# Optimization experiments

Hardware: AMD Instinct MI355X
Metric: run time of the kernel (lower is better)

## Reference

```python
import jax, jax.numpy as jnp
import numpy as np
from jax import lax

SOS_TOKEN = 2  # prev_output initialized to [[2]] in the original module


def setup_inputs() -> dict:
    key = jax.random.key(0)
    ks = jax.random.split(key, 8)
    V, E, H, S = 32000, 512, 1024, 128
    return {
        "encoder_hn": jax.random.normal(ks[0], (1, 1, H), jnp.float32),
        "encoder_cn": jax.random.normal(ks[1], (1, 1, H), jnp.float32),
        "encoder_hidden_states": jax.random.normal(ks[2], (S, H), jnp.float32),
        "emb": jax.random.normal(ks[3], (V, E), jnp.float32) * 0.02,
        "W_ih": jax.random.normal(ks[4], (4 * H, E), jnp.float32) * 0.05,
        "W_hh": jax.random.normal(ks[5], (4 * H, H), jnp.float32) * 0.05,
        "b_ih": jnp.zeros((4 * H,), jnp.float32),
        "b_hh": jnp.zeros((4 * H,), jnp.float32),
        "W_fc": jax.random.normal(ks[6], (V, 2 * H), jnp.float32) * 0.02,
        "b_fc": jnp.zeros((V,), jnp.float32),
        "cutoff": 100,
    }


def reference(encoder_hn, encoder_cn, encoder_hidden_states, emb,
              W_ih, W_hh, b_ih, b_hh, W_fc, b_fc, cutoff):
    # Greedy sequential decode: embed -> LSTM cell -> dot attention -> concat -> fc -> log_softmax
    enc = encoder_hidden_states  # (S, H)

    def step(carry, _):
        tok, h, c = carry                       # tok: int scalar, h/c: (H,)
        x = emb[tok]                            # (E,) embedding lookup
        gates = W_ih @ x + b_ih + W_hh @ h + b_hh   # (4H,) torch LSTM gate order i,f,g,o
        i, f, g, o = jnp.split(gates, 4)
        i = jax.nn.sigmoid(i)
        f = jax.nn.sigmoid(f)
        g = jnp.tanh(g)
        o = jax.nn.sigmoid(o)
        c2 = f * c + i * g
        h2 = o * jnp.tanh(c2)
        # dot attention over encoder states
        scores = jax.nn.softmax(enc @ h2)       # (S,) softmax over seq dim
        ctx = scores @ enc                      # (H,) == enc.T @ scores
        concat = jnp.concatenate([h2, ctx])     # (2H,)
        logp = jax.nn.log_softmax(W_fc @ concat + b_fc)  # (V,)
        tok2 = jnp.argmax(logp)
        return (tok2, h2, c2), (logp, tok2)

    init = (jnp.asarray(SOS_TOKEN, jnp.int32), encoder_hn[0, 0], encoder_cn[0, 0])
    _, (preds, indices) = lax.scan(step, init, xs=None, length=int(cutoff))
    return preds, indices  # (cutoff, V), (cutoff,)
```

## Files before the change

kernel.cpp:

```cpp
#include <hip/hip_runtime.h>
#include <hip/hip_bf16.h>
#include <math.h>

#define V 32000
#define E 512
#define H 1024
#define SQ 128
#define T 100
#define NB 256
#define NTI 256
#define NTA 512
#define NTB 512
#define GROWS 16
#define FROWS 125
#define NEG_BIG (-1e30f)

typedef unsigned int u32;
typedef unsigned long long u64;

struct WS {
  float gates[4*H];
  float h[H];
  float c[2][H];
  float logits[V];
  float pmax[NB];
  float psum[NB];
  u64   pkey[NB];
};

__device__ __forceinline__ float wave_sum(float v){
  #pragma unroll
  for (int m = 32; m; m >>= 1) v += __shfl_xor(v, m, 64);
  return v;
}

__device__ __forceinline__ float dot4(float4 w, const float* v){
  return w.x*v[0] + w.y*v[1] + w.z*v[2] + w.w*v[3];
}

__global__ void __launch_bounds__(NTI) k_init(const float* __restrict__ hn,
                                              const float* __restrict__ cn,
                                              WS* __restrict__ ws){
  int tid = threadIdx.x;
  for (int j = tid; j < H; j += NTI){
    ws->h[j]    = hn[j];
    ws->c[0][j] = cn[j];
  }
  ws->pmax[tid] = NEG_BIG;
  ws->psum[tid] = 0.f;
  ws->pkey[tid] = 0ull;
}

__global__ void __launch_bounds__(NTA) k_a(const float* __restrict__ emb,
                                           const float* __restrict__ W_ih,
                                           const float* __restrict__ W_hh,
                                           const float* __restrict__ b_ih,
                                           const float* __restrict__ b_hh,
                                           WS* __restrict__ ws,
                                           float* __restrict__ out,
                                           int t){
  __shared__ float redf[NTA];
  __shared__ u64   redu[NTA];
  int b = blockIdx.x, tid = threadIdx.x;
  int wv = tid >> 6, ln = tid & 63;
  int tok = 2;

  if (t > 0){
    float mb = (tid < NB) ? ws->pmax[tid] : NEG_BIG;
    float sb = (tid < NB) ? ws->psum[tid] : 0.f;
    u64   kb = (tid < NB) ? ws->pkey[tid] : 0ull;
    redf[tid] = mb; redu[tid] = kb; __syncthreads();
    for (int o = NTA/2; o; o >>= 1){
      if (tid < o){
        redf[tid] = fmaxf(redf[tid], redf[tid+o]);
        u64 a = redu[tid], c = redu[tid+o];
        redu[tid] = (a > c) ? a : c;
      }
      __syncthreads();
    }
    float m = redf[0];
    u64 key = redu[0];
    __syncthreads();
    redf[tid] = sb * expf(mb - m); __syncthreads();
    for (int o = NTA/2; o; o >>= 1){ if (tid < o) redf[tid] += redf[tid+o]; __syncthreads(); }
    float logZ = m + logf(fmaxf(redf[0], 1e-30f));

    tok = (int)(~(u32)key);
    if ((u32)tok >= (u32)V) tok = 2;

    if (tid < FROWS){
      int row = b*FROWS + tid;
      out[(size_t)(t-1)*V + row] = ws->logits[row] - logZ;
    }
    if (b == 0 && tid == 0)
      out[(size_t)T*V + (t-1)] = (float)tok;
  }

  if (t < T){
    float xv[8], hv[16];
    {
      const float4* xp = (const float4*)(emb + (size_t)tok*E) + ln*2;
      float4 x0 = xp[0], x1 = xp[1];
      xv[0]=x0.x; xv[1]=x0.y; xv[2]=x0.z; xv[3]=x0.w;
      xv[4]=x1.x; xv[5]=x1.y; xv[6]=x1.z; xv[7]=x1.w;
      const float4* hp = (const float4*)(ws->h) + ln*4;
      float4 h0 = hp[0], h1 = hp[1], h2 = hp[2], h3 = hp[3];
      hv[0]=h0.x; hv[1]=h0.y; hv[2]=h0.z; hv[3]=h0.w;
      hv[4]=h1.x; hv[5]=h1.y; hv[6]=h1.z; hv[7]=h1.w;
      hv[8]=h2.x; hv[9]=h2.y; hv[10]=h2.z; hv[11]=h2.w;
      hv[12]=h3.x; hv[13]=h3.y; hv[14]=h3.z; hv[15]=h3.w;
    }
    int rl0 = wv*2;
    int row0 = b*GROWS + rl0, row1 = row0 + 1;
    const float4* ap0 = (const float4*)(W_ih + (size_t)row0*E) + ln*2;
    const float4* ap1 = (const float4*)(W_ih + (size_t)row1*E) + ln*2;
    const float4* wh0 = (const float4*)(W_hh + (size_t)row0*H) + ln*4;
    const float4* wh1 = (const float4*)(W_hh + (size_t)row1*H) + ln*4;
    float4 ia[2], ib[2], ha[4], hb[4];
    #pragma unroll
    for (int k = 0; k < 2; ++k) ia[k] = ap0[k];
    #pragma unroll
    for (int k = 0; k < 2; ++k) ib[k] = ap1[k];
    #pragma unroll
    for (int k = 0; k < 4; ++k) ha[k] = wh0[k];
    #pragma unroll
    for (int k = 0; k < 4; ++k) hb[k] = wh1[k];
    float acc0 = dot4(ia[0], xv) + dot4(ia[1], xv+4)
               + dot4(ha[0], hv) + dot4(ha[1], hv+4) + dot4(ha[2], hv+8) + dot4(ha[3], hv+12);
    float acc1 = dot4(ib[0], xv) + dot4(ib[1], xv+4)
               + dot4(hb[0], hv) + dot4(hb[1], hv+4) + dot4(hb[2], hv+8) + dot4(hb[3], hv+12);
    acc0 = wave_sum(acc0);
    acc1 = wave_sum(acc1);
    if (ln == 0){
      ws->gates[row0] = acc0 + b_ih[row0] + b_hh[row0];
      ws->gates[row1] = acc1 + b_ih[row1] + b_hh[row1];
    }
  }
}

__global__ void __launch_bounds__(NTB) k_b(const float* __restrict__ enc,
                                           const float* __restrict__ W_fc,
                                           const float* __restrict__ b_fc,
                                           WS* __restrict__ ws,
                                           int t){
  __shared__ float concat[2*H];
  __shared__ float sc[SQ];
  __shared__ float pw[SQ];
  __shared__ float lg[128];
  __shared__ float redf[NTB];
  __shared__ u64   redu[NTB];
  int b = blockIdx.x, tid = threadIdx.x;
  int wv = tid >> 6, ln = tid & 63;

  {
    float c2v[2], h2v[2];
    #pragma unroll
    for (int k = 0; k < 2; ++k){
      int j = tid + k*NTB;
      float gi = ws->gates[j];
      float gf = ws->gates[H + j];
      float gg = ws->gates[2*H + j];
      float go = ws->gates[3*H + j];
      float co = ws->c[t & 1][j];
      float si = 1.f/(1.f + expf(-gi));
      float sf = 1.f/(1.f + expf(-gf));
      float tg = tanhf(gg);
      float so = 1.f/(1.f + expf(-go));
      float cn = sf*co + si*tg;
      float hn = so*tanhf(cn);
      c2v[k] = cn; h2v[k] = hn;
      concat[j] = hn;
    }
    if (b == 0){
      #pragma unroll
      for (int k = 0; k < 2; ++k){
        int j = tid + k*NTB;
        ws->c[(t+1) & 1][j] = c2v[k];
        ws->h[j] = h2v[k];
      }
    }
  }
  __syncthreads();

  {
    float hv[16];
    #pragma unroll
    for (int k = 0; k < 16; ++k) hv[k] = concat[ln*16 + k];
    #pragma unroll
    for (int u = 0; u < 8; ++u){
      int s0 = wv*16 + u*2, s1 = s0 + 1;
      const float4* e0p = (const float4*)(enc + (size_t)s0*H) + ln*4;
      const float4* e1p = (const float4*)(enc + (size_t)s1*H) + ln*4;
      float4 e0[4], e1[4];
      #pragma unroll
      for (int k = 0; k < 4; ++k) e0[k] = e0p[k];
      #pragma unroll
      for (int k = 0; k < 4; ++k) e1[k] = e1p[k];
      float acc0 = dot4(e0[0], hv) + dot4(e0[1], hv+4) + dot4(e0[2], hv+8) + dot4(e0[3], hv+12);
      float acc1 = dot4(e1[0], hv) + dot4(e1[1], hv+4) + dot4(e1[2], hv+8) + dot4(e1[3], hv+12);
      acc0 = wave_sum(acc0);
      acc1 = wave_sum(acc1);
      if (ln == 0){ sc[s0] = acc0; sc[s1] = acc1; }
    }
  }
  __syncthreads();

  {
    float v = (tid < SQ) ? sc[tid] : NEG_BIG;
    redf[tid] = v; __syncthreads();
    for (int o = NTB/2; o; o >>= 1){ if (tid < o) redf[tid] = fmaxf(redf[tid], redf[tid+o]); __syncthreads(); }
    float m = redf[0]; __syncthreads();
    float e = (tid < SQ) ? expf(v - m) : 0.f;
    redf[tid] = e; __syncthreads();
    for (int o = NTB/2; o; o >>= 1){ if (tid < o) redf[tid] += redf[tid+o]; __syncthreads(); }
    float S = redf[0];
    if (tid < SQ) pw[tid] = e / S;
  }
  __syncthreads();

  {
    float a0 = 0.f, a1 = 0.f;
    const float2* eb = (const float2*)enc + tid;
    for (int s = 0; s < SQ; ++s){
      float2 e = eb[(size_t)s*(H/2)];
      float w = pw[s];
      a0 += w*e.x; a1 += w*e.y;
    }
    concat[H + tid*2 + 0] = a0;
    concat[H + tid*2 + 1] = a1;
  }
  __syncthreads();

  {
    float cv[32];
    #pragma unroll
    for (int k = 0; k < 8; ++k)
      #pragma unroll
      for (int m = 0; m < 4; ++m)
        cv[k*4 + m] = concat[k*256 + ln*4 + m];

    for (int l = wv*2; l < FROWS; l += 16){
      int l1 = (l+1 < FROWS) ? l+1 : l;
      int row0 = b*FROWS + l, row1 = b*FROWS + l1;
      const float4* wp0 = (const float4*)(W_fc + (size_t)row0*2048) + ln;
      const float4* wp1 = (const float4*)(W_fc + (size_t)row1*2048) + ln;
      float4 wb0[8], wb1[8];
      #pragma unroll
      for (int k = 0; k < 8; ++k) wb0[k] = wp0[(size_t)k*64];
      #pragma unroll
      for (int k = 0; k < 8; ++k) wb1[k] = wp1[(size_t)k*64];
      float acc0 = 0.f, acc1 = 0.f;
      #pragma unroll
      for (int k = 0; k < 8; ++k){
        acc0 += dot4(wb0[k], cv + k*4);
        acc1 += dot4(wb1[k], cv + k*4);
      }
      acc0 = wave_sum(acc0);
      acc1 = wave_sum(acc1);
      if (ln == 0){
        float a0 = acc0 + b_fc[row0];
        ws->logits[row0] = a0; lg[l] = a0;
        if (l1 != l){
          float a1 = acc1 + b_fc[row1];
          ws->logits[row1] = a1; lg[l1] = a1;
        }
      }
    }
  }
  __syncthreads();

  {
    float v = (tid < FROWS) ? lg[tid] : NEG_BIG;
    redf[tid] = v; __syncthreads();
    for (int o = NTB/2; o; o >>= 1){ if (tid < o) redf[tid] = fmaxf(redf[tid], redf[tid+o]); __syncthreads(); }
    float mb = redf[0]; __syncthreads();
    float e = (tid < FROWS) ? expf(v - mb) : 0.f;
    redf[tid] = e; __syncthreads();
    for (int o = NTB/2; o; o >>= 1){ if (tid < o) redf[tid] += redf[tid+o]; __syncthreads(); }
    float sb = redf[0];

    u64 key = 0ull;
    if (tid < FROWS){
      u32 u = __float_as_uint(v);
      u32 srt = (u >> 31) ? ~u : (u | 0x80000000u);
      key = ((u64)srt << 32) | (u32)(~(u32)(b*FROWS + tid));
    }
    redu[tid] = key; __syncthreads();
    for (int o = NTB/2; o; o >>= 1){ if (tid < o){ u64 a = redu[tid], c2 = redu[tid+o]; redu[tid] = a > c2 ? a : c2; } __syncthreads(); }

    if (tid == 0){
      ws->pmax[b] = mb;
      ws->psum[b] = sb;
      ws->pkey[b] = redu[0];
    }
  }
}

extern "C" void kernel_launch(void* const* d_in, const int* in_sizes, int n_in,
                              void* d_out, int out_size, void* d_ws, size_t ws_size,
                              hipStream_t stream){
  const float* hn   = (const float*)d_in[0];
  const float* cn   = (const float*)d_in[1];
  const float* enc  = (const float*)d_in[2];
  const float* emb  = (const float*)d_in[3];
  const float* W_ih = (const float*)d_in[4];
  const float* W_hh = (const float*)d_in[5];
  const float* b_ih = (const float*)d_in[6];
  const float* b_hh = (const float*)d_in[7];
  const float* W_fc = (const float*)d_in[8];
  const float* b_fc = (const float*)d_in[9];
  float* out = (float*)d_out;
  WS* ws = (WS*)d_ws;
  if (ws_size < sizeof(WS)) return;

  k_init<<<1, NTI, 0, stream>>>(hn, cn, ws);
  for (int t = 0; t <= T; ++t){
    k_a<<<NB, NTA, 0, stream>>>(emb, W_ih, W_hh, b_ih, b_hh, ws, out, t);
    if (t < T) k_b<<<NB, NTB, 0, stream>>>(enc, W_fc, b_fc, ws, t);
  }
}
```

Measured before the change: 7.407 ms.

## Replace shared-memory tree reductions with single-wave shuffle reductions; widen fc rows per wave

Replaces the block-wide shared-memory tree reductions (many __syncthreads barriers) in both kernels with reductions done by a single wavefront using shuffle max/sum/argmax. The fc matvec now processes four W_fc rows per wave per iteration instead of two, exposing more loads in flight, and the attention context loop gets an unroll pragma. The aim is to cut barrier and LDS latency in each of the 200 small launches. Four rows of float4 buffers per lane raise register pressure.

```diff
diff --git a/kernel.cpp b/kernel.cpp
--- a/kernel.cpp
+++ b/kernel.cpp
@@ -34,6 +34,21 @@
   return v;
 }
 
+__device__ __forceinline__ float wave_max(float v){
+  #pragma unroll
+  for (int m = 32; m; m >>= 1) v = fmaxf(v, __shfl_xor(v, m, 64));
+  return v;
+}
+
+__device__ __forceinline__ u64 wave_max_u64(u64 v){
+  #pragma unroll
+  for (int m = 32; m; m >>= 1){
+    u64 o = __shfl_xor(v, m, 64);
+    v = (o > v) ? o : v;
+  }
+  return v;
+}
+
 __device__ __forceinline__ float dot4(float4 w, const float* v){
   return w.x*v[0] + w.y*v[1] + w.z*v[2] + w.w*v[3];
 }
@@ -59,34 +74,37 @@
                                            WS* __restrict__ ws,
                                            float* __restrict__ out,
                                            int t){
-  __shared__ float redf[NTA];
-  __shared__ u64   redu[NTA];
+  __shared__ float bc_logZ;
+  __shared__ int   bc_tok;
   int b = blockIdx.x, tid = threadIdx.x;
   int wv = tid >> 6, ln = tid & 63;
   int tok = 2;
 
   if (t > 0){
-    float mb = (tid < NB) ? ws->pmax[tid] : NEG_BIG;
-    float sb = (tid < NB) ? ws->psum[tid] : 0.f;
-    u64   kb = (tid < NB) ? ws->pkey[tid] : 0ull;
-    redf[tid] = mb; redu[tid] = kb; __syncthreads();
-    for (int o = NTA/2; o; o >>= 1){
-      if (tid < o){
-        redf[tid] = fmaxf(redf[tid], redf[tid+o]);
-        u64 a = redu[tid], c = redu[tid+o];
-        redu[tid] = (a > c) ? a : c;
+    if (wv == 0){
+      float mb0 = ws->pmax[ln],       mb1 = ws->pmax[ln+64];
+      float mb2 = ws->pmax[ln+128],   mb3 = ws->pmax[ln+192];
+      float sb0 = ws->psum[ln],       sb1 = ws->psum[ln+64];
+      float sb2 = ws->psum[ln+128],   sb3 = ws->psum[ln+192];
+      u64   kb0 = ws->pkey[ln],       kb1 = ws->pkey[ln+64];
+      u64   kb2 = ws->pkey[ln+128],   kb3 = ws->pkey[ln+192];
+      float m = wave_max(fmaxf(fmaxf(mb0, mb1), fmaxf(mb2, mb3)));
+      float S = sb0*expf(mb0 - m) + sb1*expf(mb1 - m)
+              + sb2*expf(mb2 - m) + sb3*expf(mb3 - m);
+      S = wave_sum(S);
+      u64 ka = (kb0 > kb1) ? kb0 : kb1;
+      u64 kc = (kb2 > kb3) ? kb2 : kb3;
+      u64 key = wave_max_u64((ka > kc) ? ka : kc);
+      if (ln == 0){
+        bc_logZ = m + logf(fmaxf(S, 1e-30f));
+        int tk = (int)(~(u32)key);
+        if ((u32)tk >= (u32)V) tk = 2;
+        bc_tok = tk;
       }
-      __syncthreads();
-    }
-    float m = redf[0];
-    u64 key = redu[0];
+    }
     __syncthreads();
-    redf[tid] = sb * expf(mb - m); __syncthreads();
-    for (int o = NTA/2; o; o >>= 1){ if (tid < o) redf[tid] += redf[tid+o]; __syncthreads(); }
-    float logZ = m + logf(fmaxf(redf[0], 1e-30f));
-
-    tok = (int)(~(u32)key);
-    if ((u32)tok >= (u32)V) tok = 2;
+    float logZ = bc_logZ;
+    tok = bc_tok;
 
     if (tid < FROWS){
       int row = b*FROWS + tid;
@@ -147,8 +165,6 @@
   __shared__ float sc[SQ];
   __shared__ float pw[SQ];
   __shared__ float lg[128];
-  __shared__ float redf[NTB];
-  __shared__ u64   redu[NTB];
   int b = blockIdx.x, tid = threadIdx.x;
   int wv = tid >> 6, ln = tid & 63;
 
@@ -205,22 +221,20 @@
   }
   __syncthreads();
 
-  {
-    float v = (tid < SQ) ? sc[tid] : NEG_BIG;
-    redf[tid] = v; __syncthreads();
-    for (int o = NTB/2; o; o >>= 1){ if (tid < o) redf[tid] = fmaxf(redf[tid], redf[tid+o]); __syncthreads(); }
-    float m = redf[0]; __syncthreads();
-    float e = (tid < SQ) ? expf(v - m) : 0.f;
-    redf[tid] = e; __syncthreads();
-    for (int o = NTB/2; o; o >>= 1){ if (tid < o) redf[tid] += redf[tid+o]; __syncthreads(); }
-    float S = redf[0];
-    if (tid < SQ) pw[tid] = e / S;
+  if (wv == 0){
+    float v0 = sc[ln], v1 = sc[ln + 64];
+    float m = wave_max(fmaxf(v0, v1));
+    float e0 = expf(v0 - m), e1 = expf(v1 - m);
+    float S = wave_sum(e0 + e1);
+    pw[ln]      = e0 / S;
+    pw[ln + 64] = e1 / S;
   }
   __syncthreads();
 
   {
     float a0 = 0.f, a1 = 0.f;
     const float2* eb = (const float2*)enc + tid;
+    #pragma unroll 8
     for (int s = 0; s < SQ; ++s){
       float2 e = eb[(size_t)s*(H/2)];
       float w = pw[s];
@@ -239,59 +253,73 @@
       for (int m = 0; m < 4; ++m)
         cv[k*4 + m] = concat[k*256 + ln*4 + m];
 
-    for (int l = wv*2; l < FROWS; l += 16){
-      int l1 = (l+1 < FROWS) ? l+1 : l;
-      int row0 = b*FROWS + l, row1 = b*FROWS + l1;
-      const float4* wp0 = (const float4*)(W_fc + (size_t)row0*2048) + ln;
-      const float4* wp1 = (const float4*)(W_fc + (size_t)row1*2048) + ln;
-      float4 wb0[8], wb1[8];
-      #pragma unroll
-      for (int k = 0; k < 8; ++k) wb0[k] = wp0[(size_t)k*64];
-      #pragma unroll
-      for (int k = 0; k < 8; ++k) wb1[k] = wp1[(size_t)k*64];
-      float acc0 = 0.f, acc1 = 0.f;
+    #pragma unroll
+    for (int it = 0; it < 4; ++it){
+      int l = wv*4 + it*32;
+      int c0 = l,     c1 = l+1, c2 = l+2, c3 = l+3;
+      if (c1 > FROWS-1) c1 = FROWS-1;
+      if (c2 > FROWS-1) c2 = FROWS-1;
+      if (c3 > FROWS-1) c3 = FROWS-1;
+      const float4* p0 = (const float4*)(W_fc + (size_t)(b*FROWS + c0)*2048) + ln;
+      const float4* p1 = (const float4*)(W_fc + (size_t)(b*FROWS + c1)*2048) + ln;
+      const float4* p2 = (const float4*)(W_fc + (size_t)(b*FROWS + c2)*2048) + ln;
+      const float4* p3 = (const float4*)(W_fc + (size_t)(b*FROWS + c3)*2048) + ln;
+      float4 w0[8], w1[8], w2[8], w3[8];
+      #pragma unroll
+      for (int k = 0; k < 8; ++k) w0[k] = p0[(size_t)k*64];
+      #pragma unroll
+      for (int k = 0; k < 8; ++k) w1[k] = p1[(size_t)k*64];
+      #pragma unroll
+      for (int k = 0; k < 8; ++k) w2[k] = p2[(size_t)k*64];
+      #pragma unroll
+      for (int k = 0; k < 8; ++k) w3[k] = p3[(size_t)k*64];
+      float a0 = 0.f, a1 = 0.f, a2 = 0.f, a3 = 0.f;
       #pragma unroll
       for (int k = 0; k < 8; ++k){
-        acc0 += dot4(wb0[k], cv + k*4);
-        acc1 += dot4(wb1[k], cv + k*4);
+        a0 += dot4(w0[k], cv + k*4);
+        a1 += dot4(w1[k], cv + k*4);
+        a2 += dot4(w2[k], cv + k*4);
+        a3 += dot4(w3[k], cv + k*4);
       }
-      acc0 = wave_sum(acc0);
-      acc1 = wave_sum(acc1);
+      a0 = wave_sum(a0);
+      a1 = wave_sum(a1);
+      a2 = wave_sum(a2);
+      a3 = wave_sum(a3);
       if (ln == 0){
-        float a0 = acc0 + b_fc[row0];
-        ws->logits[row0] = a0; lg[l] = a0;
-        if (l1 != l){
-          float a1 = acc1 + b_fc[row1];
-          ws->logits[row1] = a1; lg[l1] = a1;
-        }
+        int row = b*FROWS + l;
+        {            float x = a0 + b_fc[row];     ws->logits[row]   = x; lg[l]   = x; }
+        if (l+1 < FROWS){ float x = a1 + b_fc[row+1]; ws->logits[row+1] = x; lg[l+1] = x; }
+        if (l+2 < FROWS){ float x = a2 + b_fc[row+2]; ws->logits[row+2] = x; lg[l+2] = x; }
+        if (l+3 < FROWS){ float x = a3 + b_fc[row+3]; ws->logits[row+3] = x; lg[l+3] = x; }
       }
     }
   }
   __syncthreads();
 
-  {
-    float v = (tid < FROWS) ? lg[tid] : NEG_BIG;
-    redf[tid] = v; __syncthreads();
-    for (int o = NTB/2; o; o >>= 1){ if (tid < o) redf[tid] = fmaxf(redf[tid], redf[tid+o]); __syncthreads(); }
-    float mb = redf[0]; __syncthreads();
-    float e = (tid < FROWS) ? expf(v - mb) : 0.f;
-    redf[tid] = e; __syncthreads();
-    for (int o = NTB/2; o; o >>= 1){ if (tid < o) redf[tid] += redf[tid+o]; __syncthreads(); }
-    float sb = redf[0];
-
-    u64 key = 0ull;
-    if (tid < FROWS){
-      u32 u = __float_as_uint(v);
+  if (wv == 0){
+    float v0 = (ln < FROWS)      ? lg[ln]      : NEG_BIG;
+    float v1 = (ln + 64 < FROWS) ? lg[ln + 64] : NEG_BIG;
+    float mb = wave_max(fmaxf(v0, v1));
+    float e  = expf(v0 - mb) + expf(v1 - mb);
+    float sb = wave_sum(e);
+
+    u64 k0 = 0ull, k1 = 0ull;
+    if (ln < FROWS){
+      u32 u = __float_as_uint(v0);
       u32 srt = (u >> 31) ? ~u : (u | 0x80000000u);
-      key = ((u64)srt << 32) | (u32)(~(u32)(b*FROWS + tid));
-    }
-    redu[tid] = key; __syncthreads();
-    for (int o = NTB/2; o; o >>= 1){ if (tid < o){ u64 a = redu[tid], c2 = redu[tid+o]; redu[tid] = a > c2 ? a : c2; } __syncthreads(); }
-
-    if (tid == 0){
+      k0 = ((u64)srt << 32) | (u32)(~(u32)(b*FROWS + ln));
+    }
+    if (ln + 64 < FROWS){
+      u32 u = __float_as_uint(v1);
+      u32 srt = (u >> 31) ? ~u : (u | 0x80000000u);
+      k1 = ((u64)srt << 32) | (u32)(~(u32)(b*FROWS + ln + 64));
+    }
+    u64 key = wave_max_u64((k0 > k1) ? k0 : k1);
+
+    if (ln == 0){
       ws->pmax[b] = mb;
       ws->psum[b] = sb;
-      ws->pkey[b] = redu[0];
+      ws->pkey[b] = key;
     }
   }
 }
```

Measured after the change: 6.899 ms. 1.07x faster.
